# Optimization experiments

Measured on AMD Instinct MI355X. Metric: run time of the kernel, lower is better.

Reference implementation:

```python
import jax, jax.numpy as jnp
import numpy as np

B, H = 128, 128          # batch_size must equal hidden_dim (see torch cat semantics)
IMG_DIM, TXT_DIM = 1024, 1024
N_EDGES = 32768


def setup_inputs() -> dict:
    key = jax.random.key(0)
    k_img, k_txt, k_e, k_w1, k_w2 = jax.random.split(key, 5)
    img_features = jax.random.normal(k_img, (B, IMG_DIM), dtype=jnp.float32)
    text_features = jax.random.normal(k_txt, (B, TXT_DIM), dtype=jnp.float32)
    # unique (source, target) edges so scatter-set is deterministic
    lin = jax.random.choice(k_e, IMG_DIM * TXT_DIM, shape=(N_EDGES,), replace=False)
    src = (lin // TXT_DIM).astype(jnp.int32)
    tgt = (lin % TXT_DIM).astype(jnp.int32)
    # causal_attention_net params: Linear(2H, H) -> ReLU -> Linear(H, 1) -> Sigmoid
    W1 = jax.random.normal(k_w1, (H, 2 * H), dtype=jnp.float32) / np.sqrt(2 * H)
    b1 = jnp.zeros((H,), dtype=jnp.float32)
    w2 = jax.random.normal(k_w2, (H,), dtype=jnp.float32) / np.sqrt(H)
    b2 = jnp.zeros((), dtype=jnp.float32)
    return {"img_features": img_features, "text_features": text_features,
            "src": src, "tgt": tgt, "W1": W1, "b1": b1, "w2": w2, "b2": b2}


def reference(img_features, text_features, src, tgt, W1, b1, w2, b2):
    batch_size, img_dim = img_features.shape
    _, text_dim = text_features.shape
    # per-edge gather of feature COLUMNS: [E, B] each -> concat [E, 2B] (B == H)
    pairs = jnp.concatenate([img_features[:, src].T, text_features[:, tgt].T], axis=1)
    h = jax.nn.relu(pairs @ W1.T + b1)           # [E, H]
    a = jax.nn.sigmoid(h @ w2 + b2)              # [E] scalar attention per edge
    # scatter into dense sparse-pattern attention matrix, broadcast over batch
    A = jnp.zeros((batch_size, img_dim, text_dim), dtype=img_features.dtype)
    A = A.at[:, src, tgt].set(a)                 # [B, I, T]
    attended_img = jnp.einsum('bit,bt->bi', A, text_features)   # [B, I]
    attended_text = jnp.einsum('bit,bi->bt', A, img_features)   # [B, T]
    return (attended_img, attended_text)
```

## Files before the change

kernel.cpp:

```cpp
#include <hip/hip_runtime.h>
#include <math.h>

#define BD   128
#define NCOL 1024
#define NE   32768
#define CAP  128

__global__ __launch_bounds__(256) void prep_kernel(
    const float* __restrict__ img, const float* __restrict__ text,
    const float* __restrict__ W1, const float* __restrict__ b1,
    float* __restrict__ HimgT, float* __restrict__ HtxtT,
    float* __restrict__ imgT, float* __restrict__ textT)
{
    __shared__ __align__(16) float Wl[64 * 129];
    __shared__ __align__(16) float Sl[128 * 8];
    const int blk = blockIdx.x, tid = threadIdx.x;

    if (blk < 256) {
        const int side = blk >> 7;
        const int i0 = (blk & 127) * 8;
        const float* S = side ? text : img;
        float* Dst = side ? HtxtT : HimgT;
        const int soff = side * 128;

        {
            int b = tid >> 1, q = tid & 1;
            ((float4*)Sl)[tid] = *(const float4*)(S + b * 1024 + i0 + q * 4);
        }
        const int h = tid & 127, iq = tid >> 7;
        float acc[4] = {0.f, 0.f, 0.f, 0.f};
        #pragma unroll
        for (int half = 0; half < 2; half++) {
            __syncthreads();
            for (int idx = tid; idx < 8192; idx += 256) {
                int hh = idx >> 6, bb = idx & 63;
                Wl[bb * 129 + hh] = W1[hh * 256 + soff + half * 64 + bb];
            }
            __syncthreads();
            #pragma unroll 8
            for (int bb = 0; bb < 64; bb++) {
                int b = half * 64 + bb;
                float w = Wl[bb * 129 + h];
                float4 s4 = *(const float4*)(Sl + b * 8 + iq * 4);
                acc[0] += s4.x * w; acc[1] += s4.y * w;
                acc[2] += s4.z * w; acc[3] += s4.w * w;
            }
        }
        float bias = side ? 0.f : b1[h];
        #pragma unroll
        for (int r = 0; r < 4; r++)
            Dst[(i0 + iq * 4 + r) * 128 + h] = acc[r] + bias;
    } else {
        float (*lds)[33] = (float(*)[33])Wl;
        const int t = blk - 256;
        const float* S = (t < 128) ? img : text;
        float* D = (t < 128) ? imgT : textT;
        const int tile = t & 127;
        const int rt = tile >> 5, ct = tile & 31;
        const int x = tid & 31, y = tid >> 5;
        #pragma unroll
        for (int k = 0; k < 4; k++) {
            int r = y + k * 8;
            lds[r][x] = S[(rt * 32 + r) * 1024 + ct * 32 + x];
        }
        __syncthreads();
        #pragma unroll
        for (int k = 0; k < 4; k++) {
            int r = y + k * 8;
            D[(ct * 32 + r) * 128 + rt * 32 + x] = lds[x][r];
        }
    }
}

__global__ __launch_bounds__(256) void edge_kernel(
    const int* __restrict__ src, const int* __restrict__ tgt,
    const float* __restrict__ HimgT, const float* __restrict__ HtxtT,
    const float* __restrict__ w2, const float* __restrict__ b2,
    float* __restrict__ a_e,
    int* __restrict__ cnt_src, int* __restrict__ cnt_tgt,
    int* __restrict__ list_src, int* __restrict__ list_tgt)
{
    const int lane = threadIdx.x & 63;
    const int wgid = blockIdx.x * 4 + (threadIdx.x >> 6);
    const float w2a = w2[lane], w2b = w2[lane + 64];
    const float b2v = b2[0];
    #pragma unroll
    for (int k = 0; k < 4; k++) {
        int e = wgid * 4 + k;
        int s0 = src[e], t0 = tgt[e];
        const float* Hi = HimgT + s0 * 128;
        const float* Ht = HtxtT + t0 * 128;
        float v1 = Hi[lane]      + Ht[lane];
        float v2 = Hi[lane + 64] + Ht[lane + 64];
        float x = fmaxf(v1, 0.f) * w2a + fmaxf(v2, 0.f) * w2b;
        #pragma unroll
        for (int off = 32; off > 0; off >>= 1)
            x += __shfl_xor(x, off, 64);
        if (lane == 0) {
            a_e[e] = 1.f / (1.f + expf(-(x + b2v)));
            int p = atomicAdd(&cnt_src[s0], 1);
            if (p < CAP) list_src[s0 * CAP + p] = e;
            int q = atomicAdd(&cnt_tgt[t0], 1);
            if (q < CAP) list_tgt[t0 * CAP + q] = e;
        }
    }
}

__global__ __launch_bounds__(128) void gather_kernel(
    const int* __restrict__ src, const int* __restrict__ tgt,
    const float* __restrict__ a_e,
    const int* __restrict__ cnt_src, const int* __restrict__ cnt_tgt,
    const int* __restrict__ list_src, const int* __restrict__ list_tgt,
    const float* __restrict__ imgT, const float* __restrict__ textT,
    float* __restrict__ out)
{
    __shared__ float avl[CAP];
    __shared__ int   ol[CAP];
    const int blk = blockIdx.x, b = threadIdx.x;
    const int side = blk >> 10, c = blk & 1023;
    int n = side ? cnt_tgt[c] : cnt_src[c];
    n = min(n, CAP);
    const int* lst = (side ? list_tgt : list_src) + c * CAP;
    const int* oth = side ? src : tgt;
    const float* T = side ? imgT : textT;

    if (b < n) {
        int e = lst[b];
        ol[b]  = oth[e];
        avl[b] = a_e[e];
    }
    __syncthreads();

    float acc = 0.f;
    for (int p = 0; p < n; p++)
        acc += avl[p] * T[ol[p] * 128 + b];

    out[side * (BD * NCOL) + b * 1024 + c] = acc;
}

extern "C" void kernel_launch(void* const* d_in, const int* in_sizes, int n_in,
                              void* d_out, int out_size, void* d_ws, size_t ws_size,
                              hipStream_t stream)
{
    const float* img  = (const float*)d_in[0];
    const float* text = (const float*)d_in[1];
    const int*   src  = (const int*)  d_in[2];
    const int*   tgt  = (const int*)  d_in[3];
    const float* W1   = (const float*)d_in[4];
    const float* b1   = (const float*)d_in[5];
    const float* w2   = (const float*)d_in[6];
    const float* b2   = (const float*)d_in[7];
    float* out = (float*)d_out;

    float* HimgT   = (float*)d_ws;
    float* HtxtT   = HimgT + 131072;
    float* imgT    = HtxtT + 131072;
    float* textT   = imgT  + 131072;
    float* a_e     = textT + 131072;
    int* cnt_src   = (int*)(a_e + 32768);
    int* cnt_tgt   = cnt_src + 1024;
    int* list_src  = cnt_tgt + 1024;
    int* list_tgt  = list_src + 1024 * CAP;

    hipMemsetAsync(cnt_src, 0, 2 * 1024 * sizeof(int), stream);
    prep_kernel<<<512, 256, 0, stream>>>(img, text, W1, b1,
                                         HimgT, HtxtT, imgT, textT);
    edge_kernel<<<2048, 256, 0, stream>>>(src, tgt, HimgT, HtxtT, w2, b2,
                                          a_e, cnt_src, cnt_tgt,
                                          list_src, list_tgt);
    gather_kernel<<<2048, 128, 0, stream>>>(src, tgt, a_e,
                                            cnt_src, cnt_tgt,
                                            list_src, list_tgt,
                                            imgT, textT, out);
}
```

Baseline: 99.55 us.

## Fuse prep, edge and gather kernels into one persistent kernel with grid barriers

```diff
diff --git a/kernel.cpp b/kernel.cpp
--- a/kernel.cpp
+++ b/kernel.cpp
@@ -5,12 +5,35 @@
 #define NCOL 1024
 #define NE   32768
 #define CAP  128
+#define NBLK 1024
+#define CNT_STRIDE 16
 
-__global__ __launch_bounds__(256) void prep_kernel(
+__device__ __forceinline__ void gsync(int* bar, int target)
+{
+    __syncthreads();
+    if (threadIdx.x == 0) {
+        __threadfence();
+        __hip_atomic_fetch_add(bar, 1, __ATOMIC_RELAXED, __HIP_MEMORY_SCOPE_AGENT);
+        int spins = 0;
+        while (__hip_atomic_load(bar, __ATOMIC_RELAXED, __HIP_MEMORY_SCOPE_AGENT) < target) {
+            __builtin_amdgcn_s_sleep(8);
+            if (++spins > (1 << 20)) break;
+        }
+        __threadfence();
+    }
+    __syncthreads();
+}
+
+__global__ __launch_bounds__(256, 4) void fused_kernel(
     const float* __restrict__ img, const float* __restrict__ text,
+    const int* __restrict__ src, const int* __restrict__ tgt,
     const float* __restrict__ W1, const float* __restrict__ b1,
+    const float* __restrict__ w2, const float* __restrict__ b2,
     float* __restrict__ HimgT, float* __restrict__ HtxtT,
-    float* __restrict__ imgT, float* __restrict__ textT)
+    float* __restrict__ imgT, float* __restrict__ textT,
+    float* __restrict__ a_e, int* __restrict__ cnt,
+    int* __restrict__ list_src, int* __restrict__ list_tgt,
+    int* __restrict__ bar, float* __restrict__ out)
 {
     __shared__ __align__(16) float Wl[64 * 129];
     __shared__ __align__(16) float Sl[128 * 8];
@@ -50,7 +73,7 @@
         #pragma unroll
         for (int r = 0; r < 4; r++)
             Dst[(i0 + iq * 4 + r) * 128 + h] = acc[r] + bias;
-    } else {
+    } else if (blk < 512) {
         float (*lds)[33] = (float(*)[33])Wl;
         const int t = blk - 256;
         const float* S = (t < 128) ? img : text;
@@ -69,73 +92,72 @@
             int r = y + k * 8;
             D[(ct * 32 + r) * 128 + rt * 32 + x] = lds[x][r];
         }
+    } else if (blk < 640) {
+        cnt[(blk - 512) * 256 + tid] = 0;
     }
-}
 
-__global__ __launch_bounds__(256) void edge_kernel(
-    const int* __restrict__ src, const int* __restrict__ tgt,
-    const float* __restrict__ HimgT, const float* __restrict__ HtxtT,
-    const float* __restrict__ w2, const float* __restrict__ b2,
-    float* __restrict__ a_e,
-    int* __restrict__ cnt_src, int* __restrict__ cnt_tgt,
-    int* __restrict__ list_src, int* __restrict__ list_tgt)
-{
-    const int lane = threadIdx.x & 63;
-    const int wgid = blockIdx.x * 4 + (threadIdx.x >> 6);
-    const float w2a = w2[lane], w2b = w2[lane + 64];
-    const float b2v = b2[0];
-    #pragma unroll
-    for (int k = 0; k < 4; k++) {
-        int e = wgid * 4 + k;
-        int s0 = src[e], t0 = tgt[e];
-        const float* Hi = HimgT + s0 * 128;
-        const float* Ht = HtxtT + t0 * 128;
-        float v1 = Hi[lane]      + Ht[lane];
-        float v2 = Hi[lane + 64] + Ht[lane + 64];
-        float x = fmaxf(v1, 0.f) * w2a + fmaxf(v2, 0.f) * w2b;
+    gsync(bar, NBLK);
+
+    {
+        const int lane = tid & 63;
+        const int w = blk * 4 + (tid >> 6);
+        const float w2a = w2[lane], w2b = w2[lane + 64];
+        const float b2v = b2[0];
+        int sa[8], ta[8];
         #pragma unroll
-        for (int off = 32; off > 0; off >>= 1)
-            x += __shfl_xor(x, off, 64);
-        if (lane == 0) {
-            a_e[e] = 1.f / (1.f + expf(-(x + b2v)));
-            int p = atomicAdd(&cnt_src[s0], 1);
-            if (p < CAP) list_src[s0 * CAP + p] = e;
-            int q = atomicAdd(&cnt_tgt[t0], 1);
-            if (q < CAP) list_tgt[t0 * CAP + q] = e;
+        for (int k = 0; k < 8; k++) {
+            int e = w * 8 + k;
+            int s0 = src[e], t0 = tgt[e];
+            sa[k] = s0; ta[k] = t0;
+            const float* Hi = HimgT + s0 * 128;
+            const float* Ht = HtxtT + t0 * 128;
+            float v1 = Hi[lane]      + Ht[lane];
+            float v2 = Hi[lane + 64] + Ht[lane + 64];
+            float x = fmaxf(v1, 0.f) * w2a + fmaxf(v2, 0.f) * w2b;
+            #pragma unroll
+            for (int off = 32; off > 0; off >>= 1)
+                x += __shfl_xor(x, off, 64);
+            if (lane == 0)
+                a_e[e] = 1.f / (1.f + expf(-(x + b2v)));
+        }
+        #pragma unroll
+        for (int k = 0; k < 8; k++) {
+            int e = w * 8 + k;
+            if (lane == 0) {
+                int p = atomicAdd(&cnt[sa[k] * CNT_STRIDE], 1);
+                if (p < CAP) list_src[sa[k] * CAP + p] = e;
+            } else if (lane == 1) {
+                int q = atomicAdd(&cnt[(1024 + ta[k]) * CNT_STRIDE], 1);
+                if (q < CAP) list_tgt[ta[k] * CAP + q] = e;
+            }
         }
     }
-}
 
-__global__ __launch_bounds__(128) void gather_kernel(
-    const int* __restrict__ src, const int* __restrict__ tgt,
-    const float* __restrict__ a_e,
-    const int* __restrict__ cnt_src, const int* __restrict__ cnt_tgt,
-    const int* __restrict__ list_src, const int* __restrict__ list_tgt,
-    const float* __restrict__ imgT, const float* __restrict__ textT,
-    float* __restrict__ out)
-{
-    __shared__ float avl[CAP];
-    __shared__ int   ol[CAP];
-    const int blk = blockIdx.x, b = threadIdx.x;
-    const int side = blk >> 10, c = blk & 1023;
-    int n = side ? cnt_tgt[c] : cnt_src[c];
-    n = min(n, CAP);
-    const int* lst = (side ? list_tgt : list_src) + c * CAP;
-    const int* oth = side ? src : tgt;
-    const float* T = side ? imgT : textT;
+    gsync(bar, 2 * NBLK);
 
-    if (b < n) {
-        int e = lst[b];
-        ol[b]  = oth[e];
-        avl[b] = a_e[e];
+    {
+        float* avl = Wl;
+        int*   ol  = (int*)(Wl + 2 * CAP);
+        const int half = tid >> 7, b = tid & 127;
+        const int task = blk * 2 + half;
+        const int side = task >> 10, c = task & 1023;
+        int n = cnt[task * CNT_STRIDE];
+        n = min(n, CAP);
+        const int* lst = (side ? list_tgt : list_src) + c * CAP;
+        const int* oth = side ? src : tgt;
+        const float* T = side ? imgT : textT;
+        if (b < n) {
+            int e = lst[b];
+            ol[half * CAP + b]  = oth[e];
+            avl[half * CAP + b] = a_e[e];
+        }
+        __syncthreads();
+        float acc = 0.f;
+        #pragma unroll 4
+        for (int p = 0; p < n; p++)
+            acc += avl[half * CAP + p] * T[ol[half * CAP + p] * 128 + b];
+        out[side * (BD * NCOL) + b * 1024 + c] = acc;
     }
-    __syncthreads();
-
-    float acc = 0.f;
-    for (int p = 0; p < n; p++)
-        acc += avl[p] * T[ol[p] * 128 + b];
-
-    out[side * (BD * NCOL) + b * 1024 + c] = acc;
 }
 
 extern "C" void kernel_launch(void* const* d_in, const int* in_sizes, int n_in,
@@ -152,24 +174,19 @@
     const float* b2   = (const float*)d_in[7];
     float* out = (float*)d_out;
 
-    float* HimgT   = (float*)d_ws;
-    float* HtxtT   = HimgT + 131072;
-    float* imgT    = HtxtT + 131072;
-    float* textT   = imgT  + 131072;
-    float* a_e     = textT + 131072;
-    int* cnt_src   = (int*)(a_e + 32768);
-    int* cnt_tgt   = cnt_src + 1024;
-    int* list_src  = cnt_tgt + 1024;
-    int* list_tgt  = list_src + 1024 * CAP;
+    float* HimgT  = (float*)d_ws;
+    float* HtxtT  = HimgT + 131072;
+    float* imgT   = HtxtT + 131072;
+    float* textT  = imgT  + 131072;
+    float* a_e    = textT + 131072;
+    int* cnt      = (int*)(a_e + 32768);
+    int* list_src = cnt + 2048 * CNT_STRIDE;
+    int* list_tgt = list_src + 1024 * CAP;
+    int* bar      = list_tgt + 1024 * CAP;
 
-    hipMemsetAsync(cnt_src, 0, 2 * 1024 * sizeof(int), stream);
-    prep_kernel<<<512, 256, 0, stream>>>(img, text, W1, b1,
-                                         HimgT, HtxtT, imgT, textT);
-    edge_kernel<<<2048, 256, 0, stream>>>(src, tgt, HimgT, HtxtT, w2, b2,
-                                          a_e, cnt_src, cnt_tgt,
-                                          list_src, list_tgt);
-    gather_kernel<<<2048, 128, 0, stream>>>(src, tgt, a_e,
-                                            cnt_src, cnt_tgt,
-                                            list_src, list_tgt,
-                                            imgT, textT, out);
+    hipMemsetAsync(bar, 0, sizeof(int), stream);
+    fused_kernel<<<NBLK, 256, 0, stream>>>(img, text, src, tgt, W1, b1, w2, b2,
+                                           HimgT, HtxtT, imgT, textT,
+                                           a_e, cnt, list_src, list_tgt,
+                                           bar, out);
 }
```

After: 306.5 us. +207.9%, slower.

## Move edge bucketing into prep kernel and process four edges per wavefront

Applied to the files above, without the earlier changes.

```diff
diff --git a/kernel.cpp b/kernel.cpp
--- a/kernel.cpp
+++ b/kernel.cpp
@@ -5,12 +5,16 @@
 #define NCOL 1024
 #define NE   32768
 #define CAP  128
+#define CNT_STRIDE 16
 
 __global__ __launch_bounds__(256) void prep_kernel(
     const float* __restrict__ img, const float* __restrict__ text,
+    const int* __restrict__ src, const int* __restrict__ tgt,
     const float* __restrict__ W1, const float* __restrict__ b1,
     float* __restrict__ HimgT, float* __restrict__ HtxtT,
-    float* __restrict__ imgT, float* __restrict__ textT)
+    float* __restrict__ imgT, float* __restrict__ textT,
+    int* __restrict__ cnt,
+    int* __restrict__ list_src, int* __restrict__ list_tgt)
 {
     __shared__ __align__(16) float Wl[64 * 129];
     __shared__ __align__(16) float Sl[128 * 8];
@@ -50,7 +54,7 @@
         #pragma unroll
         for (int r = 0; r < 4; r++)
             Dst[(i0 + iq * 4 + r) * 128 + h] = acc[r] + bias;
-    } else {
+    } else if (blk < 512) {
         float (*lds)[33] = (float(*)[33])Wl;
         const int t = blk - 256;
         const float* S = (t < 128) ? img : text;
@@ -69,6 +73,13 @@
             int r = y + k * 8;
             D[(ct * 32 + r) * 128 + rt * 32 + x] = lds[x][r];
         }
+    } else {
+        const int e = (blk - 512) * 256 + tid;
+        const int s0 = src[e], t0 = tgt[e];
+        int p = atomicAdd(&cnt[s0 * CNT_STRIDE], 1);
+        if (p < CAP) list_src[s0 * CAP + p] = e;
+        int q = atomicAdd(&cnt[(1024 + t0) * CNT_STRIDE], 1);
+        if (q < CAP) list_tgt[t0 * CAP + q] = e;
     }
 }
 
@@ -76,40 +87,44 @@
     const int* __restrict__ src, const int* __restrict__ tgt,
     const float* __restrict__ HimgT, const float* __restrict__ HtxtT,
     const float* __restrict__ w2, const float* __restrict__ b2,
-    float* __restrict__ a_e,
-    int* __restrict__ cnt_src, int* __restrict__ cnt_tgt,
-    int* __restrict__ list_src, int* __restrict__ list_tgt)
+    float* __restrict__ a_e)
 {
     const int lane = threadIdx.x & 63;
-    const int wgid = blockIdx.x * 4 + (threadIdx.x >> 6);
-    const float w2a = w2[lane], w2b = w2[lane + 64];
+    const int u = lane & 15, sub = lane >> 4;
+    const int wid = blockIdx.x * 4 + (threadIdx.x >> 6);
+    const float4 wa = *(const float4*)(w2 + u * 8);
+    const float4 wb = *(const float4*)(w2 + u * 8 + 4);
     const float b2v = b2[0];
+
     #pragma unroll
-    for (int k = 0; k < 4; k++) {
-        int e = wgid * 4 + k;
-        int s0 = src[e], t0 = tgt[e];
-        const float* Hi = HimgT + s0 * 128;
-        const float* Ht = HtxtT + t0 * 128;
-        float v1 = Hi[lane]      + Ht[lane];
-        float v2 = Hi[lane + 64] + Ht[lane + 64];
-        float x = fmaxf(v1, 0.f) * w2a + fmaxf(v2, 0.f) * w2b;
+    for (int j = 0; j < 2; j++) {
+        const int e = wid * 8 + j * 4 + sub;
+        const int s0 = src[e], t0 = tgt[e];
+        const float4* Hi = (const float4*)(HimgT + s0 * 128) + u * 2;
+        const float4* Ht = (const float4*)(HtxtT + t0 * 128) + u * 2;
+        float4 h0 = Hi[0], h1 = Hi[1];
+        float4 g0 = Ht[0], g1 = Ht[1];
+        float x;
+        x  = fmaxf(h0.x + g0.x, 0.f) * wa.x;
+        x += fmaxf(h0.y + g0.y, 0.f) * wa.y;
+        x += fmaxf(h0.z + g0.z, 0.f) * wa.z;
+        x += fmaxf(h0.w + g0.w, 0.f) * wa.w;
+        x += fmaxf(h1.x + g1.x, 0.f) * wb.x;
+        x += fmaxf(h1.y + g1.y, 0.f) * wb.y;
+        x += fmaxf(h1.z + g1.z, 0.f) * wb.z;
+        x += fmaxf(h1.w + g1.w, 0.f) * wb.w;
         #pragma unroll
-        for (int off = 32; off > 0; off >>= 1)
+        for (int off = 1; off < 16; off <<= 1)
             x += __shfl_xor(x, off, 64);
-        if (lane == 0) {
+        if (u == 0)
             a_e[e] = 1.f / (1.f + expf(-(x + b2v)));
-            int p = atomicAdd(&cnt_src[s0], 1);
-            if (p < CAP) list_src[s0 * CAP + p] = e;
-            int q = atomicAdd(&cnt_tgt[t0], 1);
-            if (q < CAP) list_tgt[t0 * CAP + q] = e;
-        }
     }
 }
 
 __global__ __launch_bounds__(128) void gather_kernel(
     const int* __restrict__ src, const int* __restrict__ tgt,
     const float* __restrict__ a_e,
-    const int* __restrict__ cnt_src, const int* __restrict__ cnt_tgt,
+    const int* __restrict__ cnt,
     const int* __restrict__ list_src, const int* __restrict__ list_tgt,
     const float* __restrict__ imgT, const float* __restrict__ textT,
     float* __restrict__ out)
@@ -118,7 +133,7 @@
     __shared__ int   ol[CAP];
     const int blk = blockIdx.x, b = threadIdx.x;
     const int side = blk >> 10, c = blk & 1023;
-    int n = side ? cnt_tgt[c] : cnt_src[c];
+    int n = cnt[(side * 1024 + c) * CNT_STRIDE];
     n = min(n, CAP);
     const int* lst = (side ? list_tgt : list_src) + c * CAP;
     const int* oth = side ? src : tgt;
@@ -131,11 +146,15 @@
     }
     __syncthreads();
 
-    float acc = 0.f;
-    for (int p = 0; p < n; p++)
-        acc += avl[p] * T[ol[p] * 128 + b];
+    float acc0 = 0.f, acc1 = 0.f;
+    int p = 0;
+    for (; p + 1 < n; p += 2) {
+        acc0 += avl[p]     * T[ol[p]     * 128 + b];
+        acc1 += avl[p + 1] * T[ol[p + 1] * 128 + b];
+    }
+    if (p < n) acc0 += avl[p] * T[ol[p] * 128 + b];
 
-    out[side * (BD * NCOL) + b * 1024 + c] = acc;
+    out[side * (BD * NCOL) + b * 1024 + c] = acc0 + acc1;
 }
 
 extern "C" void kernel_launch(void* const* d_in, const int* in_sizes, int n_in,
@@ -152,24 +171,21 @@
     const float* b2   = (const float*)d_in[7];
     float* out = (float*)d_out;
 
-    float* HimgT   = (float*)d_ws;
-    float* HtxtT   = HimgT + 131072;
-    float* imgT    = HtxtT + 131072;
-    float* textT   = imgT  + 131072;
-    float* a_e     = textT + 131072;
-    int* cnt_src   = (int*)(a_e + 32768);
-    int* cnt_tgt   = cnt_src + 1024;
-    int* list_src  = cnt_tgt + 1024;
-    int* list_tgt  = list_src + 1024 * CAP;
+    float* HimgT  = (float*)d_ws;
+    float* HtxtT  = HimgT + 131072;
+    float* imgT   = HtxtT + 131072;
+    float* textT  = imgT  + 131072;
+    float* a_e    = textT + 131072;
+    int* cnt      = (int*)(a_e + 32768);
+    int* list_src = cnt + 2048 * CNT_STRIDE;
+    int* list_tgt = list_src + 1024 * CAP;
 
-    hipMemsetAsync(cnt_src, 0, 2 * 1024 * sizeof(int), stream);
-    prep_kernel<<<512, 256, 0, stream>>>(img, text, W1, b1,
-                                         HimgT, HtxtT, imgT, textT);
-    edge_kernel<<<2048, 256, 0, stream>>>(src, tgt, HimgT, HtxtT, w2, b2,
-                                          a_e, cnt_src, cnt_tgt,
-                                          list_src, list_tgt);
-    gather_kernel<<<2048, 128, 0, stream>>>(src, tgt, a_e,
-                                            cnt_src, cnt_tgt,
+    hipMemsetAsync(cnt, 0, 2048 * CNT_STRIDE * sizeof(int), stream);
+    prep_kernel<<<640, 256, 0, stream>>>(img, text, src, tgt, W1, b1,
+                                         HimgT, HtxtT, imgT, textT,
+                                         cnt, list_src, list_tgt);
+    edge_kernel<<<1024, 256, 0, stream>>>(src, tgt, HimgT, HtxtT, w2, b2, a_e);
+    gather_kernel<<<2048, 128, 0, stream>>>(src, tgt, a_e, cnt,
                                             list_src, list_tgt,
                                             imgT, textT, out);
 }
```

Measured after the change: 94.43 us (median of 2 runs). 1.05x faster.
